# Optimization experiments

Hardware: AMD Instinct MI355X
Metric: run time of the kernel (lower is better)

## Reference

```python
import jax, jax.numpy as jnp
import numpy as np

CH = 512
GROUPS = 8
EPS = 1e-5


def setup_inputs() -> dict:
    key = jax.random.key(0)
    ks = jax.random.split(key, 5)
    B, C, H, W = 16, CH, 32, 32
    x = jax.random.normal(ks[0], (B, C, H, W), dtype=jnp.float32)
    # GroupNorm affine params
    norm_w = jnp.ones((C,), dtype=jnp.float32)
    norm_b = jnp.zeros((C,), dtype=jnp.float32)
    # 1x1 conv == linear over channels; store weights as [out, in]
    qkv_w = jax.random.normal(ks[1], (3 * C, C), dtype=jnp.float32) * (C ** -0.5)
    qkv_b = jnp.zeros((3 * C,), dtype=jnp.float32)
    proj_w = jax.random.normal(ks[2], (C, C), dtype=jnp.float32) * (C ** -0.5)
    proj_b = jnp.zeros((C,), dtype=jnp.float32)
    return {"x": x, "norm_w": norm_w, "norm_b": norm_b,
            "qkv_w": qkv_w, "qkv_b": qkv_b,
            "proj_w": proj_w, "proj_b": proj_b}


def _group_norm(x, w, b):
    B, C, H, W = x.shape
    g = GROUPS
    xg = x.reshape(B, g, C // g, H * W)
    mean = xg.mean(axis=(2, 3), keepdims=True)
    var = xg.var(axis=(2, 3), keepdims=True)
    xn = (xg - mean) * jax.lax.rsqrt(var + EPS)
    xn = xn.reshape(B, C, H, W)
    return xn * w[None, :, None, None] + b[None, :, None, None]


def reference(x, norm_w, norm_b, qkv_w, qkv_b, proj_w, proj_b):
    B, C, H, W = x.shape
    h = _group_norm(x, norm_w, norm_b)  # [B,C,H,W]
    hs = h.reshape(B, C, H * W)  # spatial tokens along last axis
    # 1x1 conv QKV: [3C,C] @ [B,C,N] -> [B,3C,N]
    qkv = jnp.einsum('oc,bcn->bon', qkv_w, hs) + qkv_b[None, :, None]
    q, k, v = jnp.split(qkv, 3, axis=1)  # each [B,C,N]
    scale = C ** (-0.5)
    attn = jnp.einsum('bci,bcj->bij', q, k) * scale  # [B,N,N]
    attn = jax.nn.softmax(attn, axis=-1)
    out = jnp.einsum('bij,bcj->bci', attn, v)  # [B,C,N]
    out = jnp.einsum('oc,bcn->bon', proj_w, out) + proj_b[None, :, None]
    return x + out.reshape(B, C, H, W)
```

## Files before the change

### kernel.cpp

```cpp
#include <hip/hip_runtime.h>
#include <math.h>

#define Bn   16
#define Cn   512
#define Nn   1024
#define Gn   8
#define CPG  64
#define EPSf 1e-5f

typedef short           bf16x8 __attribute__((ext_vector_type(8)));
typedef float           f32x4  __attribute__((ext_vector_type(4)));
typedef unsigned short  u16;
typedef unsigned short  u16x4  __attribute__((ext_vector_type(4)));
typedef unsigned short  u16x8  __attribute__((ext_vector_type(8)));

__device__ __forceinline__ u16 f2b(float f) {
  union { float f; unsigned u; } c; c.f = f;
  unsigned r = (c.u + 0x7FFFu + ((c.u >> 16) & 1u)) >> 16;
  return (u16)r;
}

__device__ __forceinline__ void g2l16(const void* g, void* l) {
  __builtin_amdgcn_global_load_lds(
      (const __attribute__((address_space(1))) unsigned int*)g,
      (__attribute__((address_space(3))) unsigned int*)l, 16, 0, 0);
}

__device__ __forceinline__ void gemm_core(u16* As, u16* Bs,
    const u16* __restrict__ A, size_t sA,
    const u16* __restrict__ B, size_t sB, int K, f32x4 acc[4][4]) {
  const int t = threadIdx.x;
  const int w = t >> 6, l = t & 63, quad = l >> 4, lr = l & 15;
  const int wm = (w >> 1) * 64, wn = (w & 1) * 64;

  const int ra = w * 16 + (l >> 2);
  const int p  = l & 3;
  const int q  = p ^ ((ra >> 1) & 3);
  const u16* gA0 = A + (size_t)ra * sA + q * 8;
  const u16* gA1 = A + (size_t)(ra + 64) * sA + q * 8;
  const u16* gB0 = B + (size_t)ra * sB + q * 8;
  const u16* gB1 = B + (size_t)(ra + 64) * sB + q * 8;
  u16* lA0 = As + ra * 32 + p * 8;
  u16* lA1 = As + (ra + 64) * 32 + p * 8;
  u16* lB0 = Bs + ra * 32 + p * 8;
  u16* lB1 = Bs + (ra + 64) * 32 + p * 8;

  for (int k0 = 0; k0 < K; k0 += 32) {
    __syncthreads();
    g2l16(gA0 + k0, lA0);
    g2l16(gA1 + k0, lA1);
    g2l16(gB0 + k0, lB0);
    g2l16(gB1 + k0, lB1);
    __syncthreads();
    bf16x8 af[4], bfr[4];
    #pragma unroll
    for (int fm = 0; fm < 4; fm++) {
      int r = wm + fm * 16 + lr;
      af[fm] = *(const bf16x8*)&As[r * 32 + ((quad ^ ((r >> 1) & 3)) << 3)];
    }
    #pragma unroll
    for (int fn = 0; fn < 4; fn++) {
      int r = wn + fn * 16 + lr;
      bfr[fn] = *(const bf16x8*)&Bs[r * 32 + ((quad ^ ((r >> 1) & 3)) << 3)];
    }
    #pragma unroll
    for (int fm = 0; fm < 4; fm++)
      #pragma unroll
      for (int fn = 0; fn < 4; fn++)
        acc[fm][fn] = __builtin_amdgcn_mfma_f32_16x16x32_bf16(
            af[fm], bfr[fn], acc[fm][fn], 0, 0, 0);
  }
}

#define GEMM_PRE()                                              \
  const int t = threadIdx.x;                                    \
  const int w = t >> 6, l = t & 63, quad = l >> 4, lr = l & 15; \
  const int wm = (w >> 1) * 64, wn = (w & 1) * 64;              \
  (void)w; (void)wm; (void)wn;                                  \
  f32x4 acc[4][4];                                              \
  { f32x4 z = {0.f, 0.f, 0.f, 0.f};                             \
    for (int i_ = 0; i_ < 4; i_++)                              \
      for (int j_ = 0; j_ < 4; j_++) acc[i_][j_] = z; }

__global__ __launch_bounds__(256) void prep_k(const float* __restrict__ qkv_w,
    const float* __restrict__ proj_w, const float* __restrict__ qkv_b,
    const float* __restrict__ x, u16* __restrict__ wqk16,
    u16* __restrict__ wvT16, u16* __restrict__ pw16,
    float* __restrict__ bias2, float* __restrict__ stats) {
  __shared__ u16 T[64][68];
  __shared__ float sm[4], sq[4];
  int bid = blockIdx.x, t = threadIdx.x;
  if (bid < 512) {
    int i = bid * 256 + t;
    float4 v = ((const float4*)qkv_w)[i];
    u16x4 o;
    o.x = f2b(v.x); o.y = f2b(v.y); o.z = f2b(v.z); o.w = f2b(v.w);
    ((u16x4*)wqk16)[i] = o;
  } else if (bid < 576) {
    int tile = bid - 512, tx = tile & 7, ty = tile >> 3;
    int row = t >> 4, col4 = t & 15;
    #pragma unroll
    for (int it = 0; it < 4; it++) {
      int cc = row + it * 16;
      float4 v = *(const float4*)&qkv_w[(size_t)(1024 + ty * 64 + cc) * 512 + tx * 64 + col4 * 4];
      u16x4 o;
      o.x = f2b(v.x); o.y = f2b(v.y); o.z = f2b(v.z); o.w = f2b(v.w);
      *(u16x4*)&T[cc][col4 * 4] = o;
    }
    __syncthreads();
    #pragma unroll
    for (int it = 0; it < 2; it++) {
      int ch = t + it * 256;
      int d = ch >> 3, c8 = (ch & 7) * 8;
      u16x8 o;
      #pragma unroll
      for (int j = 0; j < 8; j++) o[j] = T[c8 + j][d];
      *(u16x8*)&wvT16[(size_t)(tx * 64 + d) * 512 + ty * 64 + c8] = o;
    }
  } else if (bid < 578) {
    int m = (bid - 576) * 256 + t;
    float s = 0.f;
    for (int c = 0; c < 512; c++)
      s += proj_w[(size_t)m * 512 + c] * qkv_b[1024 + c];
    bias2[m] = s;
  } else if (bid < 706) {
    int bg = bid - 578;
    const float4* xp = (const float4*)(x + (size_t)bg * (CPG * Nn));
    float s = 0.f, ss = 0.f;
    const int cnt4 = CPG * Nn / 4;
    for (int i = t; i < cnt4; i += 256) {
      float4 v = xp[i];
      s  += v.x + v.y + v.z + v.w;
      ss += v.x * v.x + v.y * v.y + v.z * v.z + v.w * v.w;
    }
    #pragma unroll
    for (int off = 32; off > 0; off >>= 1) {
      s  += __shfl_down(s, off);
      ss += __shfl_down(ss, off);
    }
    int lane = t & 63, wid = t >> 6;
    if (lane == 0) { sm[wid] = s; sq[wid] = ss; }
    __syncthreads();
    if (t == 0) {
      float S  = sm[0] + sm[1] + sm[2] + sm[3];
      float SS = sq[0] + sq[1] + sq[2] + sq[3];
      const float inv = 1.0f / (float)(CPG * Nn);
      float m = S * inv;
      float var = SS * inv - m * m;
      stats[bg]       = m;
      stats[128 + bg] = rsqrtf(var + EPSf);
    }
  } else {
    int i = (bid - 706) * 256 + t;
    float4 v = ((const float4*)proj_w)[i];
    u16x4 o;
    o.x = f2b(v.x); o.y = f2b(v.y); o.z = f2b(v.z); o.w = f2b(v.w);
    ((u16x4*)pw16)[i] = o;
  }
}

__global__ __launch_bounds__(256) void gnw2_k(const float* __restrict__ x,
    const float* __restrict__ stats, const float* __restrict__ nw,
    const float* __restrict__ nb, const u16* __restrict__ pw16,
    const u16* __restrict__ wvT16, u16* __restrict__ W2, u16* __restrict__ hT) {
  __shared__ u16 AsBs[8192];
  int bid = blockIdx.x;
  if (bid < 16) {
    int m0 = (bid >> 2) * 128, d0 = (bid & 3) * 128;
    GEMM_PRE();
    gemm_core(AsBs, AsBs + 4096, pw16 + (size_t)m0 * 512, 512,
              wvT16 + (size_t)d0 * 512, 512, 512, acc);
    #pragma unroll
    for (int fm = 0; fm < 4; fm++) {
      int m = m0 + wm + fm * 16 + quad * 4;
      #pragma unroll
      for (int fn = 0; fn < 4; fn++) {
        int d = d0 + wn + fn * 16 + lr;
        f32x4 a = acc[fm][fn];
        W2[(size_t)(m    ) * 512 + d] = f2b(a[0]);
        W2[(size_t)(m + 1) * 512 + d] = f2b(a[1]);
        W2[(size_t)(m + 2) * 512 + d] = f2b(a[2]);
        W2[(size_t)(m + 3) * 512 + d] = f2b(a[3]);
      }
    }
    return;
  }
  int u = bid - 16;
  int b = u >> 7, rem = u & 127, c0 = (rem >> 4) * 64, n0 = (rem & 15) * 64;
  u16 (*T)[68] = (u16(*)[68])AsBs;
  int t = threadIdx.x;
  int row = t >> 4, col4 = t & 15;
  #pragma unroll
  for (int it = 0; it < 4; it++) {
    int cc = row + it * 16;
    int c  = c0 + cc;
    int bg = b * Gn + (c >> 6);
    float mean = stats[bg], rstd = stats[128 + bg];
    float a  = nw[c] * rstd;
    float bb = nb[c] - mean * a;
    float4 xv = *(const float4*)&x[((size_t)(b * Cn + c)) * Nn + n0 + col4 * 4];
    u16x4 o;
    o.x = f2b(xv.x * a + bb); o.y = f2b(xv.y * a + bb);
    o.z = f2b(xv.z * a + bb); o.w = f2b(xv.w * a + bb);
    *(u16x4*)&T[cc][col4 * 4] = o;
  }
  __syncthreads();
  #pragma unroll
  for (int it = 0; it < 2; it++) {
    int ch = t + it * 256;
    int n  = ch >> 3, c8 = (ch & 7) * 8;
    u16x8 o;
    #pragma unroll
    for (int j = 0; j < 8; j++) o[j] = T[c8 + j][n];
    *(u16x8*)&hT[((size_t)(b * Nn + n0 + n)) * 512 + c0 + c8] = o;
  }
}

__global__ __launch_bounds__(256) void qkvp_k(const u16* __restrict__ wqk16,
    const u16* __restrict__ W2, const u16* __restrict__ hT,
    const float* __restrict__ qkv_b, u16* __restrict__ qkT,
    u16* __restrict__ VP) {
  __shared__ u16 AsBs[8192];
  int u = blockIdx.x;
  GEMM_PRE();
  if (u < 1024) {
    int b = u >> 6, rem = u & 63, m0 = (rem >> 3) * 128, n0 = (rem & 7) * 128;
    gemm_core(AsBs, AsBs + 4096, wqk16 + (size_t)m0 * 512, 512,
              hT + ((size_t)(b * Nn + n0)) * 512, 512, 512, acc);
    #pragma unroll
    for (int fm = 0; fm < 4; fm++) {
      int mb = m0 + wm + fm * 16 + quad * 4;
      float b0 = qkv_b[mb], b1 = qkv_b[mb + 1], b2 = qkv_b[mb + 2], b3 = qkv_b[mb + 3];
      #pragma unroll
      for (int fn = 0; fn < 4; fn++) {
        int n = n0 + wn + fn * 16 + lr;
        f32x4 a = acc[fm][fn];
        u16x4 o;
        o.x = f2b(a[0] + b0); o.y = f2b(a[1] + b1);
        o.z = f2b(a[2] + b2); o.w = f2b(a[3] + b3);
        *(u16x4*)&qkT[((size_t)(b * Nn + n)) * 1024 + mb] = o;
      }
    }
  } else {
    int u2 = u - 1024;
    int b = u2 >> 5, rem = u2 & 31, m0 = (rem >> 3) * 128, j0 = (rem & 7) * 128;
    gemm_core(AsBs, AsBs + 4096, W2 + (size_t)m0 * 512, 512,
              hT + ((size_t)(b * Nn + j0)) * 512, 512, 512, acc);
    #pragma unroll
    for (int fm = 0; fm < 4; fm++) {
      int m = m0 + wm + fm * 16 + quad * 4;
      #pragma unroll
      for (int fn = 0; fn < 4; fn++) {
        int j = j0 + wn + fn * 16 + lr;
        f32x4 a = acc[fm][fn];
        VP[((size_t)(b * 512 + m    )) * 1024 + j] = f2b(a[0]);
        VP[((size_t)(b * 512 + m + 1)) * 1024 + j] = f2b(a[1]);
        VP[((size_t)(b * 512 + m + 2)) * 1024 + j] = f2b(a[2]);
        VP[((size_t)(b * 512 + m + 3)) * 1024 + j] = f2b(a[3]);
      }
    }
  }
}

__global__ __launch_bounds__(256) void qkexp_k(const u16* __restrict__ qkT,
    u16* __restrict__ Pm, float* __restrict__ rpart) {
  __shared__ u16 AsBs[8192];
  __shared__ float psum[128];
  int u = blockIdx.x;
  int b = u >> 6, rem = u & 63, i0 = (rem >> 3) * 128, j0 = (rem & 7) * 128;
  const u16* base = qkT + (size_t)b * Nn * 1024;
  GEMM_PRE();
  gemm_core(AsBs, AsBs + 4096, base + (size_t)i0 * 1024, 1024,
            base + (size_t)j0 * 1024 + 512, 1024, 512, acc);
  if (t < 128) psum[t] = 0.f;
  __syncthreads();
  const float scale = 0.04419417382415922f;
  #pragma unroll
  for (int fm = 0; fm < 4; fm++) {
    int ri = wm + fm * 16 + quad * 4;
    float rs0 = 0.f, rs1 = 0.f, rs2 = 0.f, rs3 = 0.f;
    #pragma unroll
    for (int fn = 0; fn < 4; fn++) {
      int j = j0 + wn + fn * 16 + lr;
      f32x4 a = acc[fm][fn];
      float p0 = __expf(a[0] * scale);
      float p1 = __expf(a[1] * scale);
      float p2 = __expf(a[2] * scale);
      float p3 = __expf(a[3] * scale);
      u16* Pp = &Pm[((size_t)(b * Nn + i0 + ri)) * 1024 + j];
      Pp[0]    = f2b(p0);
      Pp[1024] = f2b(p1);
      Pp[2048] = f2b(p2);
      Pp[3072] = f2b(p3);
      rs0 += p0; rs1 += p1; rs2 += p2; rs3 += p3;
    }
    #pragma unroll
    for (int mask = 1; mask < 16; mask <<= 1) {
      rs0 += __shfl_xor(rs0, mask);
      rs1 += __shfl_xor(rs1, mask);
      rs2 += __shfl_xor(rs2, mask);
      rs3 += __shfl_xor(rs3, mask);
    }
    if (lr == 0) {
      atomicAdd(&psum[ri],     rs0);
      atomicAdd(&psum[ri + 1], rs1);
      atomicAdd(&psum[ri + 2], rs2);
      atomicAdd(&psum[ri + 3], rs3);
    }
  }
  __syncthreads();
  if (t < 128)
    rpart[((size_t)(b * 8) + (rem & 7)) * 1024 + i0 + t] = psum[t];
}

__global__ __launch_bounds__(256) void pvout_k(const u16* __restrict__ VP,
    const u16* __restrict__ Pm, const float* __restrict__ rpart,
    const float* __restrict__ bias2, const float* __restrict__ proj_b,
    const float* __restrict__ x, float* __restrict__ out) {
  __shared__ u16 AsBs[8192];
  __shared__ float rinv[128];
  int bid = blockIdx.x;
  int b = bid >> 5, rem = bid & 31, m0 = (rem >> 3) * 128, i0 = (rem & 7) * 128;
  if (threadIdx.x < 128) {
    float s = 0.f;
    #pragma unroll
    for (int jb = 0; jb < 8; jb++)
      s += rpart[((size_t)(b * 8 + jb)) * 1024 + i0 + threadIdx.x];
    rinv[threadIdx.x] = 1.0f / s;
  }
  GEMM_PRE();
  gemm_core(AsBs, AsBs + 4096, VP + ((size_t)(b * 512 + m0)) * 1024, 1024,
            Pm + ((size_t)(b * Nn + i0)) * 1024, 1024, 1024, acc);
  #pragma unroll
  for (int fm = 0; fm < 4; fm++) {
    int m = m0 + wm + fm * 16 + quad * 4;
    float c0 = bias2[m    ] + proj_b[m    ];
    float c1 = bias2[m + 1] + proj_b[m + 1];
    float c2 = bias2[m + 2] + proj_b[m + 2];
    float c3 = bias2[m + 3] + proj_b[m + 3];
    #pragma unroll
    for (int fn = 0; fn < 4; fn++) {
      int il = wn + fn * 16 + lr;
      int i  = i0 + il;
      float ri = rinv[il];
      f32x4 a = acc[fm][fn];
      size_t o0 = ((size_t)(b * Cn + m)) * Nn + i;
      out[o0                  ] = a[0] * ri + c0 + x[o0                  ];
      out[o0 + Nn             ] = a[1] * ri + c1 + x[o0 + Nn             ];
      out[o0 + 2 * Nn         ] = a[2] * ri + c2 + x[o0 + 2 * Nn         ];
      out[o0 + 3 * (size_t)Nn] = a[3] * ri + c3 + x[o0 + 3 * (size_t)Nn];
    }
  }
}

extern "C" void kernel_launch(void* const* d_in, const int* in_sizes, int n_in,
                              void* d_out, int out_size, void* d_ws, size_t ws_size,
                              hipStream_t stream) {
  const float* x      = (const float*)d_in[0];
  const float* norm_w = (const float*)d_in[1];
  const float* norm_b = (const float*)d_in[2];
  const float* qkv_w  = (const float*)d_in[3];
  const float* qkv_b  = (const float*)d_in[4];
  const float* proj_w = (const float*)d_in[5];
  const float* proj_b = (const float*)d_in[6];
  float* out = (float*)d_out;
  char* ws = (char*)d_ws;

  u16*   wqk16 = (u16*)(ws);
  u16*   wvT16 = (u16*)(ws + 1048576);
  u16*   pw16  = (u16*)(ws + 1572864);
  u16*   W2    = (u16*)(ws + 2097152);
  float* bias2 = (float*)(ws + 2621440);
  float* stats = (float*)(ws + 2623488);
  u16*   hT    = (u16*)(ws + 2624512);
  u16*   qkT   = (u16*)(ws + 19401728);
  u16*   VP    = (u16*)(ws + 52956160);
  u16*   Pm    = (u16*)(ws + 69733376);
  float* rpart = (float*)(ws + 103287808);

  prep_k<<<962, 256, 0, stream>>>(qkv_w, proj_w, qkv_b, x, wqk16, wvT16, pw16, bias2, stats);
  gnw2_k<<<2064, 256, 0, stream>>>(x, stats, norm_w, norm_b, pw16, wvT16, W2, hT);
  qkvp_k<<<1536, 256, 0, stream>>>(wqk16, W2, hT, qkv_b, qkT, VP);
  qkexp_k<<<1024, 256, 0, stream>>>(qkT, Pm, rpart);
  pvout_k<<<512, 256, 0, stream>>>(VP, Pm, rpart, bias2, proj_b, x, out);
}
```

Measured before the change: 242.5 us.

## Fuse five stage kernels into one cooperative persistent kernel with grid syncs

Refactors each stage kernel body into a device function and adds a persistent cooperative kernel with 512 blocks. The blocks loop over each stage's work units and separate stages with grid-wide syncs. This removes four kernel launch boundaries and their tail gaps. It adds grid-barrier cost, fixes parallelism at 512 blocks, and keeps the multi-kernel path as a fallback if cooperative launch is unavailable.

```diff
diff --git a/kernel.cpp b/kernel.cpp
--- a/kernel.cpp
+++ b/kernel.cpp
@@ -1,12 +1,16 @@
 #include <hip/hip_runtime.h>
+#include <hip/hip_cooperative_groups.h>
 #include <math.h>
 
-#define Bn   16
-#define Cn   512
-#define Nn   1024
-#define Gn   8
-#define CPG  64
-#define EPSf 1e-5f
+namespace cg = cooperative_groups;
+
+#define Bn    16
+#define Cn    512
+#define Nn    1024
+#define Gn    8
+#define CPG   64
+#define EPSf  1e-5f
+#define GRIDC 512
 
 typedef short           bf16x8 __attribute__((ext_vector_type(8)));
 typedef float           f32x4  __attribute__((ext_vector_type(4)));
@@ -76,28 +80,29 @@
   const int t = threadIdx.x;                                    \
   const int w = t >> 6, l = t & 63, quad = l >> 4, lr = l & 15; \
   const int wm = (w >> 1) * 64, wn = (w & 1) * 64;              \
-  (void)w; (void)wm; (void)wn;                                  \
+  (void)w; (void)wm; (void)wn; (void)l;                         \
   f32x4 acc[4][4];                                              \
   { f32x4 z = {0.f, 0.f, 0.f, 0.f};                             \
     for (int i_ = 0; i_ < 4; i_++)                              \
       for (int j_ = 0; j_ < 4; j_++) acc[i_][j_] = z; }
 
-__global__ __launch_bounds__(256) void prep_k(const float* __restrict__ qkv_w,
-    const float* __restrict__ proj_w, const float* __restrict__ qkv_b,
-    const float* __restrict__ x, u16* __restrict__ wqk16,
-    u16* __restrict__ wvT16, u16* __restrict__ pw16,
-    float* __restrict__ bias2, float* __restrict__ stats) {
-  __shared__ u16 T[64][68];
-  __shared__ float sm[4], sq[4];
-  int bid = blockIdx.x, t = threadIdx.x;
-  if (bid < 512) {
-    int i = bid * 256 + t;
+
+__device__ __forceinline__ void prep_unit(int u,
+    const float* __restrict__ qkv_w, const float* __restrict__ proj_w,
+    const float* __restrict__ qkv_b, const float* __restrict__ x,
+    u16* __restrict__ wqk16, u16* __restrict__ wvT16, u16* __restrict__ pw16,
+    float* __restrict__ bias2, float* __restrict__ stats,
+    u16* lds, float* redf) {
+  int t = threadIdx.x;
+  if (u < 512) {
+    int i = u * 256 + t;
     float4 v = ((const float4*)qkv_w)[i];
     u16x4 o;
     o.x = f2b(v.x); o.y = f2b(v.y); o.z = f2b(v.z); o.w = f2b(v.w);
     ((u16x4*)wqk16)[i] = o;
-  } else if (bid < 576) {
-    int tile = bid - 512, tx = tile & 7, ty = tile >> 3;
+  } else if (u < 576) {
+    u16 (*T)[68] = (u16(*)[68])lds;
+    int tile = u - 512, tx = tile & 7, ty = tile >> 3;
     int row = t >> 4, col4 = t & 15;
     #pragma unroll
     for (int it = 0; it < 4; it++) {
@@ -117,14 +122,14 @@
       for (int j = 0; j < 8; j++) o[j] = T[c8 + j][d];
       *(u16x8*)&wvT16[(size_t)(tx * 64 + d) * 512 + ty * 64 + c8] = o;
     }
-  } else if (bid < 578) {
-    int m = (bid - 576) * 256 + t;
+  } else if (u < 578) {
+    int m = (u - 576) * 256 + t;
     float s = 0.f;
     for (int c = 0; c < 512; c++)
       s += proj_w[(size_t)m * 512 + c] * qkv_b[1024 + c];
     bias2[m] = s;
-  } else if (bid < 706) {
-    int bg = bid - 578;
+  } else if (u < 706) {
+    int bg = u - 578;
     const float4* xp = (const float4*)(x + (size_t)bg * (CPG * Nn));
     float s = 0.f, ss = 0.f;
     const int cnt4 = CPG * Nn / 4;
@@ -139,11 +144,11 @@
       ss += __shfl_down(ss, off);
     }
     int lane = t & 63, wid = t >> 6;
-    if (lane == 0) { sm[wid] = s; sq[wid] = ss; }
+    if (lane == 0) { redf[wid] = s; redf[4 + wid] = ss; }
     __syncthreads();
     if (t == 0) {
-      float S  = sm[0] + sm[1] + sm[2] + sm[3];
-      float SS = sq[0] + sq[1] + sq[2] + sq[3];
+      float S  = redf[0] + redf[1] + redf[2] + redf[3];
+      float SS = redf[4] + redf[5] + redf[6] + redf[7];
       const float inv = 1.0f / (float)(CPG * Nn);
       float m = S * inv;
       float var = SS * inv - m * m;
@@ -151,7 +156,7 @@
       stats[128 + bg] = rsqrtf(var + EPSf);
     }
   } else {
-    int i = (bid - 706) * 256 + t;
+    int i = (u - 706) * 256 + t;
     float4 v = ((const float4*)proj_w)[i];
     u16x4 o;
     o.x = f2b(v.x); o.y = f2b(v.y); o.z = f2b(v.z); o.w = f2b(v.w);
@@ -159,14 +164,13 @@
   }
 }
 
-__global__ __launch_bounds__(256) void gnw2_k(const float* __restrict__ x,
+__device__ __forceinline__ void gnw2_unit(int u, const float* __restrict__ x,
     const float* __restrict__ stats, const float* __restrict__ nw,
     const float* __restrict__ nb, const u16* __restrict__ pw16,
-    const u16* __restrict__ wvT16, u16* __restrict__ W2, u16* __restrict__ hT) {
-  __shared__ u16 AsBs[8192];
-  int bid = blockIdx.x;
-  if (bid < 16) {
-    int m0 = (bid >> 2) * 128, d0 = (bid & 3) * 128;
+    const u16* __restrict__ wvT16, u16* __restrict__ W2, u16* __restrict__ hT,
+    u16* AsBs) {
+  if (u < 16) {
+    int m0 = (u >> 2) * 128, d0 = (u & 3) * 128;
     GEMM_PRE();
     gemm_core(AsBs, AsBs + 4096, pw16 + (size_t)m0 * 512, 512,
               wvT16 + (size_t)d0 * 512, 512, 512, acc);
@@ -185,8 +189,8 @@
     }
     return;
   }
-  int u = bid - 16;
-  int b = u >> 7, rem = u & 127, c0 = (rem >> 4) * 64, n0 = (rem & 15) * 64;
+  int u2 = u - 16;
+  int b = u2 >> 7, rem = u2 & 127, c0 = (rem >> 4) * 64, n0 = (rem & 15) * 64;
   u16 (*T)[68] = (u16(*)[68])AsBs;
   int t = threadIdx.x;
   int row = t >> 4, col4 = t & 15;
@@ -216,12 +220,10 @@
   }
 }
 
-__global__ __launch_bounds__(256) void qkvp_k(const u16* __restrict__ wqk16,
+__device__ __forceinline__ void qkvp_unit(int u, const u16* __restrict__ wqk16,
     const u16* __restrict__ W2, const u16* __restrict__ hT,
     const float* __restrict__ qkv_b, u16* __restrict__ qkT,
-    u16* __restrict__ VP) {
-  __shared__ u16 AsBs[8192];
-  int u = blockIdx.x;
+    u16* __restrict__ VP, u16* AsBs) {
   GEMM_PRE();
   if (u < 1024) {
     int b = u >> 6, rem = u & 63, m0 = (rem >> 3) * 128, n0 = (rem & 7) * 128;
@@ -262,11 +264,8 @@
   }
 }
 
-__global__ __launch_bounds__(256) void qkexp_k(const u16* __restrict__ qkT,
-    u16* __restrict__ Pm, float* __restrict__ rpart) {
-  __shared__ u16 AsBs[8192];
-  __shared__ float psum[128];
-  int u = blockIdx.x;
+__device__ __forceinline__ void qkexp_unit(int u, const u16* __restrict__ qkT,
+    u16* __restrict__ Pm, float* __restrict__ rpart, u16* AsBs, float* psum) {
   int b = u >> 6, rem = u & 63, i0 = (rem >> 3) * 128, j0 = (rem & 7) * 128;
   const u16* base = qkT + (size_t)b * Nn * 1024;
   GEMM_PRE();
@@ -313,14 +312,12 @@
     rpart[((size_t)(b * 8) + (rem & 7)) * 1024 + i0 + t] = psum[t];
 }
 
-__global__ __launch_bounds__(256) void pvout_k(const u16* __restrict__ VP,
+__device__ __forceinline__ void pvout_unit(int u, const u16* __restrict__ VP,
     const u16* __restrict__ Pm, const float* __restrict__ rpart,
     const float* __restrict__ bias2, const float* __restrict__ proj_b,
-    const float* __restrict__ x, float* __restrict__ out) {
-  __shared__ u16 AsBs[8192];
-  __shared__ float rinv[128];
-  int bid = blockIdx.x;
-  int b = bid >> 5, rem = bid & 31, m0 = (rem >> 3) * 128, i0 = (rem & 7) * 128;
+    const float* __restrict__ x, float* __restrict__ out,
+    u16* AsBs, float* rinv) {
+  int b = u >> 5, rem = u & 31, m0 = (rem >> 3) * 128, i0 = (rem & 7) * 128;
   if (threadIdx.x < 128) {
     float s = 0.f;
     #pragma unroll
@@ -351,6 +348,74 @@
       out[o0 + 3 * (size_t)Nn] = a[3] * ri + c3 + x[o0 + 3 * (size_t)Nn];
     }
   }
+}
+
+__global__ __launch_bounds__(256) void prep_k(const float* qkv_w,
+    const float* proj_w, const float* qkv_b, const float* x, u16* wqk16,
+    u16* wvT16, u16* pw16, float* bias2, float* stats) {
+  __shared__ u16 lds[4352];
+  __shared__ float redf[8];
+  prep_unit(blockIdx.x, qkv_w, proj_w, qkv_b, x, wqk16, wvT16, pw16, bias2,
+            stats, lds, redf);
+}
+
+__global__ __launch_bounds__(256) void gnw2_k(const float* x,
+    const float* stats, const float* nw, const float* nb, const u16* pw16,
+    const u16* wvT16, u16* W2, u16* hT) {
+  __shared__ u16 AsBs[8192];
+  gnw2_unit(blockIdx.x, x, stats, nw, nb, pw16, wvT16, W2, hT, AsBs);
+}
+
+__global__ __launch_bounds__(256) void qkvp_k(const u16* wqk16, const u16* W2,
+    const u16* hT, const float* qkv_b, u16* qkT, u16* VP) {
+  __shared__ u16 AsBs[8192];
+  qkvp_unit(blockIdx.x, wqk16, W2, hT, qkv_b, qkT, VP, AsBs);
+}
+
+__global__ __launch_bounds__(256) void qkexp_k(const u16* qkT, u16* Pm,
+                                               float* rpart) {
+  __shared__ u16 AsBs[8192];
+  __shared__ float psum[128];
+  qkexp_unit(blockIdx.x, qkT, Pm, rpart, AsBs, psum);
+}
+
+__global__ __launch_bounds__(256) void pvout_k(const u16* VP, const u16* Pm,
+    const float* rpart, const float* bias2, const float* proj_b,
+    const float* x, float* out) {
+  __shared__ u16 AsBs[8192];
+  __shared__ float rinv[128];
+  pvout_unit(blockIdx.x, VP, Pm, rpart, bias2, proj_b, x, out, AsBs, rinv);
+}
+
+__global__ __launch_bounds__(256, 2) void mega_k(
+    const float* x, const float* norm_w, const float* norm_b,
+    const float* qkv_w, const float* qkv_b, const float* proj_w,
+    const float* proj_b, float* out,
+    u16* wqk16, u16* wvT16, u16* pw16, u16* W2, float* bias2, float* stats,
+    u16* hT, u16* qkT, u16* VP, u16* Pm, float* rpart) {
+  cg::grid_group grd = cg::this_grid();
+  __shared__ u16 AsBs[8192];
+  __shared__ float redf[128];
+  const int bid = blockIdx.x;
+
+  for (int u = bid; u < 962; u += GRIDC) {
+    __syncthreads();
+    prep_unit(u, qkv_w, proj_w, qkv_b, x, wqk16, wvT16, pw16, bias2, stats,
+              AsBs, redf);
+  }
+  grd.sync();
+  for (int u = bid; u < 2064; u += GRIDC) {
+    __syncthreads();
+    gnw2_unit(u, x, stats, norm_w, norm_b, pw16, wvT16, W2, hT, AsBs);
+  }
+  grd.sync();
+  for (int u = bid; u < 1536; u += GRIDC)
+    qkvp_unit(u, wqk16, W2, hT, qkv_b, qkT, VP, AsBs);
+  grd.sync();
+  for (int u = bid; u < 1024; u += GRIDC)
+    qkexp_unit(u, qkT, Pm, rpart, AsBs, redf);
+  grd.sync();
+  pvout_unit(bid, VP, Pm, rpart, bias2, proj_b, x, out, AsBs, redf);
 }
 
 extern "C" void kernel_launch(void* const* d_in, const int* in_sizes, int n_in,
@@ -378,9 +443,32 @@
   u16*   Pm    = (u16*)(ws + 69733376);
   float* rpart = (float*)(ws + 103287808);
 
-  prep_k<<<962, 256, 0, stream>>>(qkv_w, proj_w, qkv_b, x, wqk16, wvT16, pw16, bias2, stats);
-  gnw2_k<<<2064, 256, 0, stream>>>(x, stats, norm_w, norm_b, pw16, wvT16, W2, hT);
-  qkvp_k<<<1536, 256, 0, stream>>>(wqk16, W2, hT, qkv_b, qkT, VP);
-  qkexp_k<<<1024, 256, 0, stream>>>(qkT, Pm, rpart);
-  pvout_k<<<512, 256, 0, stream>>>(VP, Pm, rpart, bias2, proj_b, x, out);
-}
+  int dev = 0;
+  (void)hipGetDevice(&dev);
+  int coopAttr = 0, nCU = 0, maxB = 0;
+  (void)hipDeviceGetAttribute(&coopAttr, hipDeviceAttributeCooperativeLaunch, dev);
+  (void)hipDeviceGetAttribute(&nCU, hipDeviceAttributeMultiprocessorCount, dev);
+  (void)hipOccupancyMaxActiveBlocksPerMultiprocessor(&maxB, (const void*)mega_k,
+                                                     256, 0);
+  hipError_t err = hipErrorUnknown;
+  if (coopAttr && maxB > 0 && (long)maxB * nCU >= GRIDC) {
+    void* args[] = {
+      (void*)&x, (void*)&norm_w, (void*)&norm_b, (void*)&qkv_w, (void*)&qkv_b,
+      (void*)&proj_w, (void*)&proj_b, (void*)&out,
+      (void*)&wqk16, (void*)&wvT16, (void*)&pw16, (void*)&W2, (void*)&bias2,
+      (void*)&stats, (void*)&hT, (void*)&qkT, (void*)&VP, (void*)&Pm,
+      (void*)&rpart,
+    };
+    err = hipLaunchCooperativeKernel((const void*)mega_k, dim3(GRIDC),
+                                     dim3(256), args, 0, stream);
+  }
+  if (err != hipSuccess) {
+    prep_k<<<962, 256, 0, stream>>>(qkv_w, proj_w, qkv_b, x, wqk16, wvT16,
+                                    pw16, bias2, stats);
+    gnw2_k<<<2064, 256, 0, stream>>>(x, stats, norm_w, norm_b, pw16, wvT16,
+                                     W2, hT);
+    qkvp_k<<<1536, 256, 0, stream>>>(wqk16, W2, hT, qkv_b, qkT, VP);
+    qkexp_k<<<1024, 256, 0, stream>>>(qkT, Pm, rpart);
+    pvout_k<<<512, 256, 0, stream>>>(VP, Pm, rpart, bias2, proj_b, x, out);
+  }
+}
```

Result: no change. 242.0 us (-0.2%).

## Stage GEMM epilogues through LDS for coalesced stores and split GroupNorm stats

Applied to the files above, without the earlier changes.

The epilogues of the QKV/VP GEMM and the QK-exp kernel now write bf16 results into a padded LDS tile in two halves and then flush them with 16-byte coalesced global stores. Previously each lane wrote scattered 2- or 8-byte values. GroupNorm statistics are now computed by four blocks per group that atomically accumulate sum and sum-of-squares, and the consumer derives mean and rstd from them. This raises parallelism in the stats phase. The cost is extra barriers, LDS traffic, a memset, and recomputing exp in the epilogue.

```diff
diff --git a/kernel.cpp b/kernel.cpp
--- a/kernel.cpp
+++ b/kernel.cpp
@@ -13,6 +13,8 @@
 typedef unsigned short  u16;
 typedef unsigned short  u16x4  __attribute__((ext_vector_type(4)));
 typedef unsigned short  u16x8  __attribute__((ext_vector_type(8)));
+
+#define TS 136
 
 __device__ __forceinline__ u16 f2b(float f) {
   union { float f; unsigned u; } c; c.f = f;
@@ -76,11 +78,22 @@
   const int t = threadIdx.x;                                    \
   const int w = t >> 6, l = t & 63, quad = l >> 4, lr = l & 15; \
   const int wm = (w >> 1) * 64, wn = (w & 1) * 64;              \
-  (void)w; (void)wm; (void)wn;                                  \
+  (void)w; (void)wm; (void)wn; (void)l;                         \
   f32x4 acc[4][4];                                              \
   { f32x4 z = {0.f, 0.f, 0.f, 0.f};                             \
     for (int i_ = 0; i_ < 4; i_++)                              \
       for (int j_ = 0; j_ < 4; j_++) acc[i_][j_] = z; }
+
+#define TILE_FLUSH(T, DST, rowstride)                           \
+  {                                                             \
+    _Pragma("unroll")                                           \
+    for (int k_ = 0; k_ < 4; k_++) {                            \
+      int idx = threadIdx.x + 256 * k_;                         \
+      int row = idx >> 4, ch = idx & 15;                        \
+      u16x8 v_ = *(u16x8*)&T[row * TS + ch * 8];                \
+      *(u16x8*)&(DST)[(size_t)row * (rowstride) + ch * 8] = v_; \
+    }                                                           \
+  }
 
 __global__ __launch_bounds__(256) void prep_k(const float* __restrict__ qkv_w,
     const float* __restrict__ proj_w, const float* __restrict__ qkv_b,
@@ -88,7 +101,7 @@
     u16* __restrict__ wvT16, u16* __restrict__ pw16,
     float* __restrict__ bias2, float* __restrict__ stats) {
   __shared__ u16 T[64][68];
-  __shared__ float sm[4], sq[4];
+  __shared__ float redf[8];
   int bid = blockIdx.x, t = threadIdx.x;
   if (bid < 512) {
     int i = bid * 256 + t;
@@ -123,12 +136,11 @@
     for (int c = 0; c < 512; c++)
       s += proj_w[(size_t)m * 512 + c] * qkv_b[1024 + c];
     bias2[m] = s;
-  } else if (bid < 706) {
-    int bg = bid - 578;
-    const float4* xp = (const float4*)(x + (size_t)bg * (CPG * Nn));
+  } else if (bid < 1090) {
+    int idx = bid - 578, bg = idx >> 2, part = idx & 3;
+    const float4* xp = (const float4*)x + (size_t)bg * 16384 + part * 4096;
     float s = 0.f, ss = 0.f;
-    const int cnt4 = CPG * Nn / 4;
-    for (int i = t; i < cnt4; i += 256) {
+    for (int i = t; i < 4096; i += 256) {
       float4 v = xp[i];
       s  += v.x + v.y + v.z + v.w;
       ss += v.x * v.x + v.y * v.y + v.z * v.z + v.w * v.w;
@@ -139,19 +151,14 @@
       ss += __shfl_down(ss, off);
     }
     int lane = t & 63, wid = t >> 6;
-    if (lane == 0) { sm[wid] = s; sq[wid] = ss; }
+    if (lane == 0) { redf[wid] = s; redf[4 + wid] = ss; }
     __syncthreads();
     if (t == 0) {
-      float S  = sm[0] + sm[1] + sm[2] + sm[3];
-      float SS = sq[0] + sq[1] + sq[2] + sq[3];
-      const float inv = 1.0f / (float)(CPG * Nn);
-      float m = S * inv;
-      float var = SS * inv - m * m;
-      stats[bg]       = m;
-      stats[128 + bg] = rsqrtf(var + EPSf);
+      atomicAdd(&stats[bg],       redf[0] + redf[1] + redf[2] + redf[3]);
+      atomicAdd(&stats[128 + bg], redf[4] + redf[5] + redf[6] + redf[7]);
     }
   } else {
-    int i = (bid - 706) * 256 + t;
+    int i = (bid - 1090) * 256 + t;
     float4 v = ((const float4*)proj_w)[i];
     u16x4 o;
     o.x = f2b(v.x); o.y = f2b(v.y); o.z = f2b(v.z); o.w = f2b(v.w);
@@ -190,12 +197,15 @@
   u16 (*T)[68] = (u16(*)[68])AsBs;
   int t = threadIdx.x;
   int row = t >> 4, col4 = t & 15;
+  const float inv = 1.0f / 65536.0f;
   #pragma unroll
   for (int it = 0; it < 4; it++) {
     int cc = row + it * 16;
     int c  = c0 + cc;
     int bg = b * Gn + (c >> 6);
-    float mean = stats[bg], rstd = stats[128 + bg];
+    float mean = stats[bg] * inv;
+    float var  = stats[128 + bg] * inv - mean * mean;
+    float rstd = rsqrtf(var + EPSf);
     float a  = nw[c] * rstd;
     float bb = nb[c] - mean * a;
     float4 xv = *(const float4*)&x[((size_t)(b * Cn + c)) * Nn + n0 + col4 * 4];
@@ -220,57 +230,81 @@
     const u16* __restrict__ W2, const u16* __restrict__ hT,
     const float* __restrict__ qkv_b, u16* __restrict__ qkT,
     u16* __restrict__ VP) {
-  __shared__ u16 AsBs[8192];
+  __shared__ u16 SH[64 * TS];
   int u = blockIdx.x;
   GEMM_PRE();
   if (u < 1024) {
     int b = u >> 6, rem = u & 63, m0 = (rem >> 3) * 128, n0 = (rem & 7) * 128;
-    gemm_core(AsBs, AsBs + 4096, wqk16 + (size_t)m0 * 512, 512,
+    gemm_core(SH, SH + 4096, wqk16 + (size_t)m0 * 512, 512,
               hT + ((size_t)(b * Nn + n0)) * 512, 512, 512, acc);
+    float bss[4][4];
     #pragma unroll
     for (int fm = 0; fm < 4; fm++) {
       int mb = m0 + wm + fm * 16 + quad * 4;
-      float b0 = qkv_b[mb], b1 = qkv_b[mb + 1], b2 = qkv_b[mb + 2], b3 = qkv_b[mb + 3];
       #pragma unroll
-      for (int fn = 0; fn < 4; fn++) {
-        int n = n0 + wn + fn * 16 + lr;
-        f32x4 a = acc[fm][fn];
-        u16x4 o;
-        o.x = f2b(a[0] + b0); o.y = f2b(a[1] + b1);
-        o.z = f2b(a[2] + b2); o.w = f2b(a[3] + b3);
-        *(u16x4*)&qkT[((size_t)(b * Nn + n)) * 1024 + mb] = o;
+      for (int r = 0; r < 4; r++) bss[fm][r] = qkv_b[mb + r];
+    }
+    #pragma unroll
+    for (int h = 0; h < 2; h++) {
+      __syncthreads();
+      if ((w & 1) == h) {
+        #pragma unroll
+        for (int fm = 0; fm < 4; fm++) {
+          int mb = wm + fm * 16 + quad * 4;
+          #pragma unroll
+          for (int fn = 0; fn < 4; fn++) {
+            int nl = fn * 16 + lr;
+            f32x4 a = acc[fm][fn];
+            u16x4 pk;
+            pk.x = f2b(a[0] + bss[fm][0]); pk.y = f2b(a[1] + bss[fm][1]);
+            pk.z = f2b(a[2] + bss[fm][2]); pk.w = f2b(a[3] + bss[fm][3]);
+            *(u16x4*)&SH[nl * TS + mb] = pk;
+          }
+        }
       }
+      __syncthreads();
+      u16* dst = qkT + ((size_t)(b * Nn + n0 + h * 64)) * 1024 + m0;
+      TILE_FLUSH(SH, dst, 1024);
     }
   } else {
     int u2 = u - 1024;
     int b = u2 >> 5, rem = u2 & 31, m0 = (rem >> 3) * 128, j0 = (rem & 7) * 128;
-    gemm_core(AsBs, AsBs + 4096, W2 + (size_t)m0 * 512, 512,
+    gemm_core(SH, SH + 4096, W2 + (size_t)m0 * 512, 512,
               hT + ((size_t)(b * Nn + j0)) * 512, 512, 512, acc);
     #pragma unroll
-    for (int fm = 0; fm < 4; fm++) {
-      int m = m0 + wm + fm * 16 + quad * 4;
-      #pragma unroll
-      for (int fn = 0; fn < 4; fn++) {
-        int j = j0 + wn + fn * 16 + lr;
-        f32x4 a = acc[fm][fn];
-        VP[((size_t)(b * 512 + m    )) * 1024 + j] = f2b(a[0]);
-        VP[((size_t)(b * 512 + m + 1)) * 1024 + j] = f2b(a[1]);
-        VP[((size_t)(b * 512 + m + 2)) * 1024 + j] = f2b(a[2]);
-        VP[((size_t)(b * 512 + m + 3)) * 1024 + j] = f2b(a[3]);
+    for (int h = 0; h < 2; h++) {
+      __syncthreads();
+      if ((w >> 1) == h) {
+        #pragma unroll
+        for (int fm = 0; fm < 4; fm++) {
+          int ml = fm * 16 + quad * 4;
+          #pragma unroll
+          for (int fn = 0; fn < 4; fn++) {
+            int jl = wn + fn * 16 + lr;
+            f32x4 a = acc[fm][fn];
+            SH[(ml    ) * TS + jl] = f2b(a[0]);
+            SH[(ml + 1) * TS + jl] = f2b(a[1]);
+            SH[(ml + 2) * TS + jl] = f2b(a[2]);
+            SH[(ml + 3) * TS + jl] = f2b(a[3]);
+          }
+        }
       }
+      __syncthreads();
+      u16* dst = VP + ((size_t)(b * 512 + m0 + h * 64)) * 1024 + j0;
+      TILE_FLUSH(SH, dst, 1024);
     }
   }
 }
 
 __global__ __launch_bounds__(256) void qkexp_k(const u16* __restrict__ qkT,
     u16* __restrict__ Pm, float* __restrict__ rpart) {
-  __shared__ u16 AsBs[8192];
+  __shared__ u16 SH[64 * TS];
   __shared__ float psum[128];
   int u = blockIdx.x;
   int b = u >> 6, rem = u & 63, i0 = (rem >> 3) * 128, j0 = (rem & 7) * 128;
   const u16* base = qkT + (size_t)b * Nn * 1024;
   GEMM_PRE();
-  gemm_core(AsBs, AsBs + 4096, base + (size_t)i0 * 1024, 1024,
+  gemm_core(SH, SH + 4096, base + (size_t)i0 * 1024, 1024,
             base + (size_t)j0 * 1024 + 512, 1024, 512, acc);
   if (t < 128) psum[t] = 0.f;
   __syncthreads();
@@ -281,18 +315,11 @@
     float rs0 = 0.f, rs1 = 0.f, rs2 = 0.f, rs3 = 0.f;
     #pragma unroll
     for (int fn = 0; fn < 4; fn++) {
-      int j = j0 + wn + fn * 16 + lr;
       f32x4 a = acc[fm][fn];
-      float p0 = __expf(a[0] * scale);
-      float p1 = __expf(a[1] * scale);
-      float p2 = __expf(a[2] * scale);
-      float p3 = __expf(a[3] * scale);
-      u16* Pp = &Pm[((size_t)(b * Nn + i0 + ri)) * 1024 + j];
-      Pp[0]    = f2b(p0);
-      Pp[1024] = f2b(p1);
-      Pp[2048] = f2b(p2);
-      Pp[3072] = f2b(p3);
-      rs0 += p0; rs1 += p1; rs2 += p2; rs3 += p3;
+      rs0 += __expf(a[0] * scale);
+      rs1 += __expf(a[1] * scale);
+      rs2 += __expf(a[2] * scale);
+      rs3 += __expf(a[3] * scale);
     }
     #pragma unroll
     for (int mask = 1; mask < 16; mask <<= 1) {
@@ -311,6 +338,28 @@
   __syncthreads();
   if (t < 128)
     rpart[((size_t)(b * 8) + (rem & 7)) * 1024 + i0 + t] = psum[t];
+  #pragma unroll
+  for (int h = 0; h < 2; h++) {
+    __syncthreads();
+    if ((w >> 1) == h) {
+      #pragma unroll
+      for (int fm = 0; fm < 4; fm++) {
+        int il = fm * 16 + quad * 4;
+        #pragma unroll
+        for (int fn = 0; fn < 4; fn++) {
+          int jl = wn + fn * 16 + lr;
+          f32x4 a = acc[fm][fn];
+          SH[(il    ) * TS + jl] = f2b(__expf(a[0] * scale));
+          SH[(il + 1) * TS + jl] = f2b(__expf(a[1] * scale));
+          SH[(il + 2) * TS + jl] = f2b(__expf(a[2] * scale));
+          SH[(il + 3) * TS + jl] = f2b(__expf(a[3] * scale));
+        }
+      }
+    }
+    __syncthreads();
+    u16* dst = Pm + ((size_t)(b * Nn + i0 + h * 64)) * 1024 + j0;
+    TILE_FLUSH(SH, dst, 1024);
+  }
 }
 
 __global__ __launch_bounds__(256) void pvout_k(const u16* __restrict__ VP,
@@ -378,8 +427,11 @@
   u16*   Pm    = (u16*)(ws + 69733376);
   float* rpart = (float*)(ws + 103287808);
 
-  prep_k<<<962, 256, 0, stream>>>(qkv_w, proj_w, qkv_b, x, wqk16, wvT16, pw16, bias2, stats);
-  gnw2_k<<<2064, 256, 0, stream>>>(x, stats, norm_w, norm_b, pw16, wvT16, W2, hT);
+  hipMemsetAsync(stats, 0, 1024, stream);
+  prep_k<<<1346, 256, 0, stream>>>(qkv_w, proj_w, qkv_b, x, wqk16, wvT16,
+                                   pw16, bias2, stats);
+  gnw2_k<<<2064, 256, 0, stream>>>(x, stats, norm_w, norm_b, pw16, wvT16,
+                                   W2, hT);
   qkvp_k<<<1536, 256, 0, stream>>>(wqk16, W2, hT, qkv_b, qkT, VP);
   qkexp_k<<<1024, 256, 0, stream>>>(qkT, Pm, rpart);
   pvout_k<<<512, 256, 0, stream>>>(VP, Pm, rpart, bias2, proj_b, x, out);
```

Result: faster. 233.4 us (-3.8%).
